# Kernel tuning notes

Measured on AMD Instinct MI355X. Metric: run time of the kernel, lower is better.

The kernel has to match this reference:

```python
import jax, jax.numpy as jnp
import numpy as np
import math

H = 8
D_MODEL = 512
D_K = D_MODEL // H


def _windows(x, r):
    # x: (b, h, t, d) -> (b, h, t, r, d) with zero padding (matches nn.Unfold)
    r2 = r // 2
    xp = jnp.pad(x, ((0, 0), (0, 0), (r2, r2), (0, 0)))
    T = x.shape[2]
    return jnp.stack([xp[:, :, j:j + T] for j in range(r)], axis=3)


def setup_inputs() -> dict:
    key = jax.random.key(0)
    ks = jax.random.split(key, 12)
    B, T = 4, 2048
    s = 1.0 / math.sqrt(D_MODEL)
    inp = {
        "query": jax.random.normal(ks[0], (B, T, D_MODEL), jnp.float32),
        "key": jax.random.normal(ks[1], (B, T, D_MODEL), jnp.float32),
        "value": jax.random.normal(ks[2], (B, T, D_MODEL), jnp.float32),
        "mask": jnp.ones((B, 1, T), jnp.int32),
        "restrict": 31,
        "Wq": jax.random.normal(ks[3], (D_MODEL, D_MODEL), jnp.float32) * s,
        "bq": jnp.zeros((D_MODEL,), jnp.float32),
        "Wk": jax.random.normal(ks[4], (D_MODEL, D_MODEL), jnp.float32) * s,
        "bk": jnp.zeros((D_MODEL,), jnp.float32),
        "Wv": jax.random.normal(ks[5], (D_MODEL, D_MODEL), jnp.float32) * s,
        "bv": jnp.zeros((D_MODEL,), jnp.float32),
        "Wo": jax.random.normal(ks[6], (D_MODEL, D_MODEL), jnp.float32) * s,
        "bo": jnp.zeros((D_MODEL,), jnp.float32),
    }
    return inp


def reference(query, key, value, mask, restrict, Wq, bq, Wk, bk, Wv, bv, Wo, bo):
    B, T, _ = query.shape
    # QKV projections -> (b, h, t, d_k)
    def proj(x, W, b):
        return (x @ W + b).reshape(B, T, H, D_K).transpose(0, 2, 1, 3)
    q = proj(query, Wq, bq)
    k = proj(key, Wk, bk)
    v = proj(value, Wv, bv)

    kwin = _windows(k, restrict)  # (b,h,t,r,d)
    vwin = _windows(v, restrict)  # (b,h,t,r,d)

    # banded scores; zero-padded edges yield score 0 (as in torch Unfold path)
    scores = jnp.einsum('bhtd,bhtjd->bhtj', q, kwin) / math.sqrt(D_K)
    attn = jax.nn.softmax(scores, axis=-1)
    # masked_fill(mask==0, 0) AFTER softmax; mask (b,1,t) broadcasts over heads
    attn = attn * (mask[:, :, :, None] != 0).astype(attn.dtype)

    x = jnp.einsum('bhtj,bhtjd->bhtd', attn, vwin)
    x = x.transpose(0, 2, 1, 3).reshape(B, T, D_MODEL)
    return x @ Wo + bo
```

## Files before the change

kernel.cpp:

```cpp
#include <hip/hip_runtime.h>

typedef unsigned short u16;
typedef unsigned int u32;

typedef __attribute__((ext_vector_type(8))) short short8;
typedef __attribute__((ext_vector_type(4))) float f32x4;

#define DEV static __device__ __forceinline__
#define GLOBAL_AS __attribute__((address_space(1)))
#define LDS_AS __attribute__((address_space(3)))

DEV u16 f2bf(float f) {
    u32 u = __float_as_uint(f);
    u += 0x7fffu + ((u >> 16) & 1u);
    return (u16)(u >> 16);
}
DEV float bflo(u32 u) { return __uint_as_float(u << 16); }
DEV float bfhi(u32 u) { return __uint_as_float(u & 0xffff0000u); }
DEV u32 pack2(float a, float b) { return (u32)f2bf(a) | ((u32)f2bf(b) << 16); }

DEV void gload16(const u16* g, u16* l) {
    __builtin_amdgcn_global_load_lds((const GLOBAL_AS u32*)(const void*)g,
                                     (LDS_AS u32*)(void*)l, 16, 0, 0);
}

__global__ __launch_bounds__(256) void cvt_kernel(
    const float* __restrict__ q, const float* __restrict__ k,
    const float* __restrict__ v, u16* __restrict__ oq,
    u16* __restrict__ ok, u16* __restrict__ ov)
{
    const float* src = (blockIdx.y == 0) ? q : (blockIdx.y == 1) ? k : v;
    u16* dst = (blockIdx.y == 0) ? oq : (blockIdx.y == 1) ? ok : ov;
    const int NCH = 8192 * 512 / 8;
    for (int i = blockIdx.x * 256 + threadIdx.x; i < NCH; i += gridDim.x * 256) {
        const float4* p = (const float4*)(src + (size_t)i * 8);
        const float4 a = p[0], b = p[1];
        uint4 o;
        o.x = pack2(a.x, a.y); o.y = pack2(a.z, a.w);
        o.z = pack2(b.x, b.y); o.w = pack2(b.z, b.w);
        *(uint4*)(dst + (size_t)i * 8) = o;
    }
}

__global__ __launch_bounds__(256) void wtrans_kernel(
    const float* __restrict__ Wq, const float* __restrict__ Wk,
    const float* __restrict__ Wv, const float* __restrict__ Wo,
    u16* __restrict__ out)
{
    __shared__ float tile[32][33];
    const float* W = (blockIdx.z == 0) ? Wq : (blockIdx.z == 1) ? Wk
                   : (blockIdx.z == 2) ? Wv : Wo;
    u16* Wt = out + (size_t)blockIdx.z * 512 * 512;
    const int n0 = blockIdx.x * 32, k0 = blockIdx.y * 32;
    const int c = threadIdx.x & 31, r0 = threadIdx.x >> 5;
#pragma unroll
    for (int i = 0; i < 4; ++i) {
        int r = r0 + i * 8;
        tile[r][c] = W[(size_t)(k0 + r) * 512 + (n0 + c)];
    }
    __syncthreads();
#pragma unroll
    for (int i = 0; i < 4; ++i) {
        int r = r0 + i * 8;
        Wt[(size_t)(n0 + r) * 512 + (k0 + c)] = f2bf(tile[c][r]);
    }
}

template<bool OUT_F32>
DEV void gemm_body(const u16* __restrict__ A, const u16* __restrict__ Wt,
                   const float* __restrict__ bias, void* __restrict__ Cptr,
                   int bm, int bn)
{
    __shared__ u16 As[128 * 64];
    __shared__ u16 Bs[128 * 64];
    const char* AsB = (const char*)As;
    const char* BsB = (const char*)Bs;

    const int tid = threadIdx.x;
    const int lane = tid & 63;
    const int wave = tid >> 6;
    const int wr = wave >> 1, wc = wave & 1;
    const int l15 = lane & 15, l4 = lane >> 4;
    const int m0 = bm * 128, n0 = bn * 128;

    const f32x4 fzero = {0.f, 0.f, 0.f, 0.f};
    f32x4 acc[4][4];
#pragma unroll
    for (int i = 0; i < 4; ++i)
#pragma unroll
        for (int j = 0; j < 4; ++j) acc[i][j] = fzero;

    for (int k0 = 0; k0 < 512; k0 += 64) {
        __syncthreads();
#pragma unroll
        for (int i = 0; i < 4; ++i) {
            const int chunk = i * 256 + tid;
            const int row = chunk >> 3;
            const int ccs = (chunk & 7) ^ (row & 7);
            gload16(A + (size_t)(m0 + row) * 512 + k0 + ccs * 8, &As[chunk * 8]);
            gload16(Wt + (size_t)(n0 + row) * 512 + k0 + ccs * 8, &Bs[chunk * 8]);
        }
        __syncthreads();

#pragma unroll
        for (int kk = 0; kk < 2; ++kk) {
            short8 af[4], bf[4];
#pragma unroll
            for (int mi = 0; mi < 4; ++mi) {
                const int row = wr * 64 + mi * 16 + l15;
                const int cc = (kk * 4 + l4) ^ (row & 7);
                af[mi] = *(const short8*)(AsB + row * 128 + cc * 16);
            }
#pragma unroll
            for (int ni = 0; ni < 4; ++ni) {
                const int row = wc * 64 + ni * 16 + l15;
                const int cc = (kk * 4 + l4) ^ (row & 7);
                bf[ni] = *(const short8*)(BsB + row * 128 + cc * 16);
            }
#pragma unroll
            for (int mi = 0; mi < 4; ++mi)
#pragma unroll
                for (int ni = 0; ni < 4; ++ni)
                    acc[mi][ni] = __builtin_amdgcn_mfma_f32_16x16x32_bf16(
                        af[mi], bf[ni], acc[mi][ni], 0, 0, 0);
        }
    }

#pragma unroll
    for (int ni = 0; ni < 4; ++ni) {
        const int n = n0 + wc * 64 + ni * 16 + l15;
        const float bv = bias[n];
#pragma unroll
        for (int mi = 0; mi < 4; ++mi) {
            const int mb = m0 + wr * 64 + mi * 16 + l4 * 4;
#pragma unroll
            for (int r = 0; r < 4; ++r) {
                const float v = acc[mi][ni][r] + bv;
                if (OUT_F32)
                    ((float*)Cptr)[(size_t)(mb + r) * 512 + n] = v;
                else
                    ((u16*)Cptr)[(size_t)(mb + r) * 512 + n] = f2bf(v);
            }
        }
    }
}

DEV void remap_block(int id, int& bm, int& bn)
{
    const int swz = (id & 7) * 32 + (id >> 3);
    bn = swz & 3;
    bm = swz >> 2;
}

__global__ __launch_bounds__(256) void gemm_qkv_kernel(
    const u16* __restrict__ qc, const u16* __restrict__ kc,
    const u16* __restrict__ vc, const u16* __restrict__ Wt3,
    const float* __restrict__ bq, const float* __restrict__ bk,
    const float* __restrict__ bv,
    u16* __restrict__ Qo, u16* __restrict__ Ko, u16* __restrict__ Vo)
{
    const int mat = blockIdx.y;
    const u16* A = (mat == 0) ? qc : (mat == 1) ? kc : vc;
    const u16* W = Wt3 + (size_t)mat * 512 * 512;
    const float* bias = (mat == 0) ? bq : (mat == 1) ? bk : bv;
    u16* C = (mat == 0) ? Qo : (mat == 1) ? Ko : Vo;
    int bm, bn; remap_block(blockIdx.x, bm, bn);
    gemm_body<false>(A, W, bias, C, bm, bn);
}

__global__ __launch_bounds__(256) void gemm_out_kernel(
    const u16* __restrict__ Xb, const u16* __restrict__ Wto,
    const float* __restrict__ bo, float* __restrict__ out)
{
    int bm, bn; remap_block(blockIdx.x, bm, bn);
    gemm_body<true>(Xb, Wto, bo, out, bm, bn);
}

__global__ __launch_bounds__(128) void attn_kernel(
    const u16* __restrict__ Qb, const u16* __restrict__ Kb,
    const u16* __restrict__ Vb, const int* __restrict__ mask,
    u16* __restrict__ Xb)
{
    constexpr int TB = 128, R2 = 15, RW = 31, WR = TB + 2 * R2;
    __shared__ u16 Ks[WR * 64];
    __shared__ u16 Vs[WR * 64];
    char* KsB = (char*)Ks;
    char* VsB = (char*)Vs;
    const int tid = threadIdx.x;
    const int blk = blockIdx.x;
    const int tb = blk & 15, h = (blk >> 4) & 7, b = blk >> 7;
    const int t0 = tb * TB;
    const size_t hbase = (size_t)b * (2048 * 512) + h * 64;

    for (int u = tid; u < WR * 8; u += 128) {
        const int r = u >> 3, c = u & 7;
        const int g = t0 - R2 + r;
        uint4 kv = make_uint4(0, 0, 0, 0), vv = make_uint4(0, 0, 0, 0);
        if (g >= 0 && g < 2048) {
            const size_t off = hbase + (size_t)g * 512 + c * 8;
            kv = *(const uint4*)(Kb + off);
            vv = *(const uint4*)(Vb + off);
        }
        const int addr = r * 128 + ((c * 16) ^ ((r & 7) << 4));
        *(uint4*)(KsB + addr) = kv;
        *(uint4*)(VsB + addr) = vv;
    }
    __syncthreads();

    const int t = t0 + tid;
    float q[64];
    {
        const uint4* qp = (const uint4*)(Qb + hbase + (size_t)t * 512);
#pragma unroll
        for (int c = 0; c < 8; ++c) {
            const uint4 u = qp[c];
            q[c*8+0] = bflo(u.x); q[c*8+1] = bfhi(u.x);
            q[c*8+2] = bflo(u.y); q[c*8+3] = bfhi(u.y);
            q[c*8+4] = bflo(u.z); q[c*8+5] = bfhi(u.z);
            q[c*8+6] = bflo(u.w); q[c*8+7] = bfhi(u.w);
        }
    }
    float x[64];
#pragma unroll
    for (int d = 0; d < 64; ++d) x[d] = 0.f;
    float m = -1e30f, sum = 0.f;

#pragma unroll 1
    for (int j = 0; j < RW; ++j) {
        const int row = tid + j;
        const int rb = row * 128, sw = (row & 7) << 4;
        uint4 kv[8];
#pragma unroll
        for (int c = 0; c < 8; ++c)
            kv[c] = *(const uint4*)(KsB + rb + ((c * 16) ^ sw));
        float a0 = 0.f, a1 = 0.f, a2 = 0.f, a3 = 0.f;
#pragma unroll
        for (int c = 0; c < 8; ++c) {
            a0 += q[c*8+0] * bflo(kv[c].x) + q[c*8+1] * bfhi(kv[c].x);
            a1 += q[c*8+2] * bflo(kv[c].y) + q[c*8+3] * bfhi(kv[c].y);
            a2 += q[c*8+4] * bflo(kv[c].z) + q[c*8+5] * bfhi(kv[c].z);
            a3 += q[c*8+6] * bflo(kv[c].w) + q[c*8+7] * bfhi(kv[c].w);
        }
        const float s = ((a0 + a1) + (a2 + a3)) * 0.125f;
        if (s > m) {
            const float sc = __expf(m - s);
            sum *= sc;
#pragma unroll
            for (int d = 0; d < 64; ++d) x[d] *= sc;
            m = s;
        }
        const float w = __expf(s - m);
        sum += w;
        uint4 vv[8];
#pragma unroll
        for (int c = 0; c < 8; ++c)
            vv[c] = *(const uint4*)(VsB + rb + ((c * 16) ^ sw));
#pragma unroll
        for (int c = 0; c < 8; ++c) {
            x[c*8+0] += w * bflo(vv[c].x); x[c*8+1] += w * bfhi(vv[c].x);
            x[c*8+2] += w * bflo(vv[c].y); x[c*8+3] += w * bfhi(vv[c].y);
            x[c*8+4] += w * bflo(vv[c].z); x[c*8+5] += w * bfhi(vv[c].z);
            x[c*8+6] += w * bflo(vv[c].w); x[c*8+7] += w * bfhi(vv[c].w);
        }
    }
    float inv = 1.0f / sum;
    if (mask[b * 2048 + t] == 0) inv = 0.f;
    u16* xp = Xb + hbase + (size_t)t * 512;
#pragma unroll
    for (int c = 0; c < 8; ++c) {
        uint4 o;
        o.x = pack2(x[c*8+0] * inv, x[c*8+1] * inv);
        o.y = pack2(x[c*8+2] * inv, x[c*8+3] * inv);
        o.z = pack2(x[c*8+4] * inv, x[c*8+5] * inv);
        o.w = pack2(x[c*8+6] * inv, x[c*8+7] * inv);
        *(uint4*)(xp + c * 8) = o;
    }
}

extern "C" void kernel_launch(void* const* d_in, const int* in_sizes, int n_in,
                              void* d_out, int out_size, void* d_ws, size_t ws_size,
                              hipStream_t stream)
{
    const float* query = (const float*)d_in[0];
    const float* key   = (const float*)d_in[1];
    const float* value = (const float*)d_in[2];
    const int*   mask  = (const int*)d_in[3];
    const float* Wq = (const float*)d_in[5];
    const float* bq = (const float*)d_in[6];
    const float* Wk = (const float*)d_in[7];
    const float* bk = (const float*)d_in[8];
    const float* Wv = (const float*)d_in[9];
    const float* bv = (const float*)d_in[10];
    const float* Wo = (const float*)d_in[11];
    const float* bo = (const float*)d_in[12];

    constexpr size_t MSZ = (size_t)8192 * 512;
    u16* wsp = (u16*)d_ws;
    u16* Wt = wsp;
    u16* qc = wsp + 4 * 512 * 512;
    u16* kc = qc + MSZ;
    u16* vc = kc + MSZ;
    u16* Qb = vc + MSZ;
    u16* Kb = Qb + MSZ;
    u16* Vb = Kb + MSZ;
    u16* Xb = qc;
    (void)in_sizes; (void)n_in; (void)out_size; (void)ws_size;

    cvt_kernel<<<dim3(1024, 3), 256, 0, stream>>>(query, key, value, qc, kc, vc);
    wtrans_kernel<<<dim3(16, 16, 4), 256, 0, stream>>>(Wq, Wk, Wv, Wo, Wt);
    gemm_qkv_kernel<<<dim3(256, 3), 256, 0, stream>>>(
        qc, kc, vc, Wt, bq, bk, bv, Qb, Kb, Vb);
    attn_kernel<<<512, 128, 0, stream>>>(Qb, Kb, Vb, mask, Xb);
    gemm_out_kernel<<<256, 256, 0, stream>>>(Xb, Wt + 3 * 512 * 512, bo,
                                             (float*)d_out);
}
```

Before: 185.5 us.

## Rewrite banded attention with MFMA tiles per wave and transposed V in LDS

```diff
diff --git a/kernel.cpp b/kernel.cpp
--- a/kernel.cpp
+++ b/kernel.cpp
@@ -176,104 +176,186 @@
     gemm_body<true>(Xb, Wto, bo, out, bm, bn);
 }
 
-__global__ __launch_bounds__(128) void attn_kernel(
+__global__ __launch_bounds__(256) void attn_kernel(
     const u16* __restrict__ Qb, const u16* __restrict__ Kb,
     const u16* __restrict__ Vb, const int* __restrict__ mask,
     u16* __restrict__ Xb)
 {
-    constexpr int TB = 128, R2 = 15, RW = 31, WR = TB + 2 * R2;
+    constexpr int TB = 128, R2 = 15, WR = 160;
+    constexpr int VS = 384;
     __shared__ u16 Ks[WR * 64];
-    __shared__ u16 Vs[WR * 64];
+    __shared__ u16 Qs[TB * 64];
+    __shared__ u16 Vt[64 * (VS / 2)];
     char* KsB = (char*)Ks;
-    char* VsB = (char*)Vs;
+    char* QsB = (char*)Qs;
+    char* VtB = (char*)Vt;
+
     const int tid = threadIdx.x;
     const int blk = blockIdx.x;
     const int tb = blk & 15, h = (blk >> 4) & 7, b = blk >> 7;
-    const int t0 = tb * TB;
+    const int T0 = tb * TB;
+    const int G0 = T0 - R2;
     const size_t hbase = (size_t)b * (2048 * 512) + h * 64;
 
-    for (int u = tid; u < WR * 8; u += 128) {
+    for (int u = tid; u < WR * 8; u += 256) {
         const int r = u >> 3, c = u & 7;
-        const int g = t0 - R2 + r;
+        const int g = G0 + r;
         uint4 kv = make_uint4(0, 0, 0, 0), vv = make_uint4(0, 0, 0, 0);
         if (g >= 0 && g < 2048) {
             const size_t off = hbase + (size_t)g * 512 + c * 8;
             kv = *(const uint4*)(Kb + off);
             vv = *(const uint4*)(Vb + off);
         }
-        const int addr = r * 128 + ((c * 16) ^ ((r & 7) << 4));
-        *(uint4*)(KsB + addr) = kv;
-        *(uint4*)(VsB + addr) = vv;
+        *(uint4*)(KsB + r * 128 + ((c ^ (r & 7)) << 4)) = kv;
+        const int cv = r >> 3, relem = r & 7;
+        const u16 vs[8] = {
+            (u16)(vv.x & 0xffff), (u16)(vv.x >> 16),
+            (u16)(vv.y & 0xffff), (u16)(vv.y >> 16),
+            (u16)(vv.z & 0xffff), (u16)(vv.z >> 16),
+            (u16)(vv.w & 0xffff), (u16)(vv.w >> 16)};
+#pragma unroll
+        for (int i = 0; i < 8; ++i) {
+            const int d = c * 8 + i;
+            const int cs = (cv & 24) | ((cv & 7) ^ (d & 7));
+            *(u16*)(VtB + d * VS + cs * 16 + relem * 2) = vs[i];
+        }
+    }
+    for (int u = tid; u < TB * 8; u += 256) {
+        const int r = u >> 3, c = u & 7;
+        const uint4 qv = *(const uint4*)(Qb + hbase + (size_t)(T0 + r) * 512 + c * 8);
+        *(uint4*)(QsB + r * 128 + ((c ^ (r & 7)) << 4)) = qv;
     }
     __syncthreads();
 
-    const int t = t0 + tid;
-    float q[64];
-    {
-        const uint4* qp = (const uint4*)(Qb + hbase + (size_t)t * 512);
-#pragma unroll
-        for (int c = 0; c < 8; ++c) {
-            const uint4 u = qp[c];
-            q[c*8+0] = bflo(u.x); q[c*8+1] = bfhi(u.x);
-            q[c*8+2] = bflo(u.y); q[c*8+3] = bfhi(u.y);
-            q[c*8+4] = bflo(u.z); q[c*8+5] = bfhi(u.z);
-            q[c*8+6] = bflo(u.w); q[c*8+7] = bfhi(u.w);
-        }
-    }
-    float x[64];
-#pragma unroll
-    for (int d = 0; d < 64; ++d) x[d] = 0.f;
-    float m = -1e30f, sum = 0.f;
-
-#pragma unroll 1
-    for (int j = 0; j < RW; ++j) {
-        const int row = tid + j;
-        const int rb = row * 128, sw = (row & 7) << 4;
-        uint4 kv[8];
-#pragma unroll
-        for (int c = 0; c < 8; ++c)
-            kv[c] = *(const uint4*)(KsB + rb + ((c * 16) ^ sw));
-        float a0 = 0.f, a1 = 0.f, a2 = 0.f, a3 = 0.f;
-#pragma unroll
-        for (int c = 0; c < 8; ++c) {
-            a0 += q[c*8+0] * bflo(kv[c].x) + q[c*8+1] * bfhi(kv[c].x);
-            a1 += q[c*8+2] * bflo(kv[c].y) + q[c*8+3] * bfhi(kv[c].y);
-            a2 += q[c*8+4] * bflo(kv[c].z) + q[c*8+5] * bfhi(kv[c].z);
-            a3 += q[c*8+6] * bflo(kv[c].w) + q[c*8+7] * bfhi(kv[c].w);
-        }
-        const float s = ((a0 + a1) + (a2 + a3)) * 0.125f;
-        if (s > m) {
-            const float sc = __expf(m - s);
-            sum *= sc;
-#pragma unroll
-            for (int d = 0; d < 64; ++d) x[d] *= sc;
-            m = s;
-        }
-        const float w = __expf(s - m);
-        sum += w;
-        uint4 vv[8];
-#pragma unroll
-        for (int c = 0; c < 8; ++c)
-            vv[c] = *(const uint4*)(VsB + rb + ((c * 16) ^ sw));
-#pragma unroll
-        for (int c = 0; c < 8; ++c) {
-            x[c*8+0] += w * bflo(vv[c].x); x[c*8+1] += w * bfhi(vv[c].x);
-            x[c*8+2] += w * bflo(vv[c].y); x[c*8+3] += w * bfhi(vv[c].y);
-            x[c*8+4] += w * bflo(vv[c].z); x[c*8+5] += w * bfhi(vv[c].z);
-            x[c*8+6] += w * bflo(vv[c].w); x[c*8+7] += w * bfhi(vv[c].w);
-        }
-    }
-    float inv = 1.0f / sum;
-    if (mask[b * 2048 + t] == 0) inv = 0.f;
-    u16* xp = Xb + hbase + (size_t)t * 512;
-#pragma unroll
-    for (int c = 0; c < 8; ++c) {
-        uint4 o;
-        o.x = pack2(x[c*8+0] * inv, x[c*8+1] * inv);
-        o.y = pack2(x[c*8+2] * inv, x[c*8+3] * inv);
-        o.z = pack2(x[c*8+4] * inv, x[c*8+5] * inv);
-        o.w = pack2(x[c*8+6] * inv, x[c*8+7] * inv);
-        *(uint4*)(xp + c * 8) = o;
+    const int lane = tid & 63;
+    const int w = tid >> 6;
+    const int l15 = lane & 15, l4 = lane >> 4;
+    const int wrow0 = w * 32;
+    char* Pw = QsB + wrow0 * 128;
+
+    short8 aq[2][2], bk_[4][2];
+#pragma unroll
+    for (int mt = 0; mt < 2; ++mt)
+#pragma unroll
+        for (int kk = 0; kk < 2; ++kk) {
+            const int r = wrow0 + mt * 16 + l15;
+            const int cc = (kk * 4 + l4) ^ (r & 7);
+            aq[mt][kk] = *(const short8*)(QsB + r * 128 + cc * 16);
+        }
+#pragma unroll
+    for (int nt = 0; nt < 4; ++nt)
+#pragma unroll
+        for (int kk = 0; kk < 2; ++kk) {
+            const int kr = wrow0 + nt * 16 + l15;
+            const int cc = (kk * 4 + l4) ^ (kr & 7);
+            bk_[nt][kk] = *(const short8*)(KsB + kr * 128 + cc * 16);
+        }
+    const f32x4 fzero = {0.f, 0.f, 0.f, 0.f};
+    f32x4 s[2][4];
+#pragma unroll
+    for (int mt = 0; mt < 2; ++mt)
+#pragma unroll
+        for (int nt = 0; nt < 4; ++nt) {
+            s[mt][nt] = fzero;
+#pragma unroll
+            for (int kk = 0; kk < 2; ++kk)
+                s[mt][nt] = __builtin_amdgcn_mfma_f32_16x16x32_bf16(
+                    aq[mt][kk], bk_[nt][kk], s[mt][nt], 0, 0, 0);
+        }
+
+    float inv_[2][4];
+#pragma unroll
+    for (int mt = 0; mt < 2; ++mt) {
+#pragma unroll
+        for (int reg = 0; reg < 4; ++reg) {
+            const int r = mt * 16 + l4 * 4 + reg;
+            float pv[4];
+            float mx = -1e30f;
+#pragma unroll
+            for (int nt = 0; nt < 4; ++nt) {
+                const int jj = nt * 16 + l15;
+                float sv = s[mt][nt][reg] * 0.125f;
+                sv = (jj >= r && jj <= r + 30) ? sv : -1e30f;
+                pv[nt] = sv;
+                mx = fmaxf(mx, sv);
+            }
+            mx = fmaxf(mx, __shfl_xor(mx, 1));
+            mx = fmaxf(mx, __shfl_xor(mx, 2));
+            mx = fmaxf(mx, __shfl_xor(mx, 4));
+            mx = fmaxf(mx, __shfl_xor(mx, 8));
+            float sum = 0.f;
+#pragma unroll
+            for (int nt = 0; nt < 4; ++nt) {
+                const float p = __expf(pv[nt] - mx);
+                pv[nt] = p;
+                sum += p;
+            }
+            sum += __shfl_xor(sum, 1);
+            sum += __shfl_xor(sum, 2);
+            sum += __shfl_xor(sum, 4);
+            sum += __shfl_xor(sum, 8);
+            inv_[mt][reg] = 1.0f / sum;
+#pragma unroll
+            for (int nt = 0; nt < 4; ++nt) {
+                const int jj = nt * 16 + l15;
+                const int cc = (jj >> 3) ^ (r & 7);
+                *(u16*)(Pw + r * 128 + cc * 16 + (jj & 7) * 2) = f2bf(pv[nt]);
+            }
+        }
+    }
+
+    short8 pa[2][2], bv[4][2];
+#pragma unroll
+    for (int mt = 0; mt < 2; ++mt)
+#pragma unroll
+        for (int kk = 0; kk < 2; ++kk) {
+            const int r = mt * 16 + l15;
+            const int cc = (kk * 4 + l4) ^ (r & 7);
+            pa[mt][kk] = *(const short8*)(Pw + r * 128 + cc * 16);
+        }
+#pragma unroll
+    for (int dt = 0; dt < 4; ++dt)
+#pragma unroll
+        for (int kk = 0; kk < 2; ++kk) {
+            const int d = dt * 16 + l15;
+            const int c = w * 4 + kk * 4 + l4;
+            const int cs = (c & 24) | ((c & 7) ^ (d & 7));
+            bv[dt][kk] = *(const short8*)(VtB + d * VS + cs * 16);
+        }
+    f32x4 o[2][4];
+#pragma unroll
+    for (int mt = 0; mt < 2; ++mt)
+#pragma unroll
+        for (int dt = 0; dt < 4; ++dt) {
+            o[mt][dt] = fzero;
+#pragma unroll
+            for (int kk = 0; kk < 2; ++kk)
+                o[mt][dt] = __builtin_amdgcn_mfma_f32_16x16x32_bf16(
+                    pa[mt][kk], bv[dt][kk], o[mt][dt], 0, 0, 0);
+        }
+
+#pragma unroll
+    for (int mt = 0; mt < 2; ++mt)
+#pragma unroll
+        for (int reg = 0; reg < 4; ++reg) {
+            const int r = mt * 16 + l4 * 4 + reg;
+            const int t = T0 + wrow0 + r;
+            float iv = inv_[mt][reg];
+            if (mask[b * 2048 + t] == 0) iv = 0.f;
+#pragma unroll
+            for (int dt = 0; dt < 4; ++dt) {
+                const int d = dt * 16 + l15;
+                const int cc = (d >> 3) ^ (r & 7);
+                *(u16*)(Pw + r * 128 + cc * 16 + (d & 7) * 2) =
+                    f2bf(o[mt][dt][reg] * iv);
+            }
+        }
+#pragma unroll
+    for (int it = 0; it < 4; ++it) {
+        const int chunk = it * 64 + lane;
+        const int r = chunk >> 3, c = chunk & 7;
+        const uint4 ov = *(const uint4*)(Pw + r * 128 + ((c ^ (r & 7)) << 4));
+        *(uint4*)(Xb + hbase + (size_t)(T0 + wrow0 + r) * 512 + c * 8) = ov;
     }
 }
 
@@ -310,7 +392,7 @@
     wtrans_kernel<<<dim3(16, 16, 4), 256, 0, stream>>>(Wq, Wk, Wv, Wo, Wt);
     gemm_qkv_kernel<<<dim3(256, 3), 256, 0, stream>>>(
         qc, kc, vc, Wt, bq, bk, bv, Qb, Kb, Vb);
-    attn_kernel<<<512, 128, 0, stream>>>(Qb, Kb, Vb, mask, Xb);
+    attn_kernel<<<512, 256, 0, stream>>>(Qb, Kb, Vb, mask, Xb);
     gemm_out_kernel<<<256, 256, 0, stream>>>(Xb, Wt + 3 * 512 * 512, bo,
                                              (float*)d_out);
 }
```

Result: faster. 155.6 us (-16.1%).
